# Kernel optimization log

Hardware: AMD Instinct MI355X
Metric: run time of the kernel (lower is better)

## Reference

```python
import jax, jax.numpy as jnp
import numpy as np

B, N = 8, 2048
D_IN, D_FEAT, H, K = 2, 30, 64, 8
D_ATT = D_IN + D_FEAT + H  # 96, per-head attention input dim
ALPHA = 0.2
NEG = -1e9


def setup_inputs() -> dict:
    key = jax.random.key(0)
    ks = jax.random.split(key, 11)
    inputs = jax.random.normal(ks[0], (B, N, D_IN), jnp.float32)
    envs_feat = jax.random.normal(ks[1], (B, N, D_FEAT), jnp.float32)
    state_t = jax.random.normal(ks[2], (B, N, H), jnp.float32)
    conn = jax.random.uniform(ks[3], (N, N)) < 0.05
    conn = conn | jnp.eye(N, dtype=bool)
    bias_mat = jnp.where(conn, 0.0, NEG).astype(jnp.float32)
    # xavier-ish init (gain 1.414)
    def xav(k, shape, fi, fo):
        lim = 1.414 * np.sqrt(6.0 / (fi + fo))
        return jax.random.uniform(k, shape, jnp.float32, -lim, lim)
    W_h = xav(ks[4], (K, D_ATT, H), D_ATT, H)      # stacked per-head W
    a1_h = xav(ks[5], (K, H), H, 1)
    a2_h = xav(ks[6], (K, H), H, 1)
    W_o = xav(ks[7], (K * H, H), K * H, H)
    a1_o = xav(ks[8], (H,), H, 1)
    a2_o = xav(ks[9], (H,), H, 1)
    return {"inputs": inputs, "envs_feat": envs_feat, "state_t": state_t,
            "bias_mat": bias_mat, "W_h": W_h, "a1_h": a1_h, "a2_h": a2_h,
            "W_o": W_o, "a1_o": a1_o, "a2_o": a2_o}


def _gat_multihead(h, bias, W, a1, a2):
    # h: [b,n,d], W: [k,d,h], a1/a2: [k,h], bias: [n,n]
    Wh = jnp.einsum('bnd,kdh->bknh', h, W)
    f1 = jnp.einsum('bknh,kh->bkn', Wh, a1)
    f2 = jnp.einsum('bknh,kh->bkn', Wh, a2)
    e = jax.nn.leaky_relu(f1[:, :, :, None] + f2[:, :, None, :], ALPHA) + bias  # [b,k,n,n]
    att = jax.nn.softmax(e, axis=-1)
    return jnp.einsum('bknm,bkmh->bknh', att, Wh)  # [b,k,n,h]


def _gat_single(h, bias, W, a1, a2):
    # h: [b,n,d], W: [d,h], a1/a2: [h]
    Wh = jnp.einsum('bnd,dh->bnh', h, W)
    f1 = Wh @ a1  # [b,n]
    f2 = Wh @ a2
    e = jax.nn.leaky_relu(f1[:, :, None] + f2[:, None, :], ALPHA) + bias  # [b,n,n]
    att = jax.nn.softmax(e, axis=-1)
    return jnp.einsum('bnm,bmh->bnh', att, Wh)


def reference(inputs, envs_feat, state_t, bias_mat, W_h, a1_h, a2_h, W_o, a1_o, a2_o):
    b, n = inputs.shape[0], inputs.shape[1]
    h = jnp.concatenate([inputs, envs_feat, state_t], axis=2)  # [b,n,D_ATT]
    hp = _gat_multihead(h, bias_mat, W_h, a1_h, a2_h)          # [b,k,n,h]
    h1 = jax.nn.elu(hp)
    h1 = jnp.transpose(h1, (0, 2, 1, 3)).reshape(b, n, -1)     # concat heads: [b,n,k*h]
    out = jax.nn.elu(_gat_single(h1, bias_mat, W_o, a1_o, a2_o))
    return out
```

## Files before the change

kernel.cpp:

```cpp
#include <hip/hip_runtime.h>
#include <hip/hip_bf16.h>
#include <math.h>

#define B   8
#define N   2048
#define DIN 2
#define DF  30
#define HH  64
#define KK  8
#define DATT 96
#define CAP 384
#define CAPL 176
#define ALPHA 0.2f

__device__ __forceinline__ float lrelu(float x) { return x > 0.f ? x : ALPHA * x; }
__device__ __forceinline__ float elu1(float x)  { return x > 0.f ? x : (__expf(x) - 1.f); }
__device__ __forceinline__ unsigned short f2bf(float x) {
    __hip_bfloat16 h = __float2bfloat16(x);
    return *reinterpret_cast<unsigned short*>(&h);
}
__device__ __forceinline__ float bflo(unsigned int u) { return __int_as_float(u << 16); }
__device__ __forceinline__ float bfhi(unsigned int u) { return __int_as_float(u & 0xffff0000u); }

__global__ void k_mask(const float* __restrict__ bias, int* __restrict__ cols,
                       int* __restrict__ cnt) {
    int i = blockIdx.x;
    int lane = threadIdx.x;
    int c = 0;
    for (int j0 = 0; j0 < N; j0 += 64) {
        float v = bias[(size_t)i * N + j0 + lane];
        bool conn = v > -1e8f;
        unsigned long long m = __ballot(conn);
        if (conn) {
            int pos = c + __popcll(m & ((1ull << lane) - 1ull));
            if (pos < CAP) cols[i * CAP + pos] = j0 + lane;
        }
        c += __popcll(m);
    }
    if (lane == 0) cnt[i] = c < CAP ? c : CAP;
}

__global__ void k_wh(const float* __restrict__ inp, const float* __restrict__ envs,
                     const float* __restrict__ st,  const float* __restrict__ W_h,
                     const float* __restrict__ a1,  const float* __restrict__ a2,
                     unsigned short* __restrict__ Whb,
                     float* __restrict__ f1n, float* __restrict__ f2n) {
    __shared__ float Ws[DATT * HH];
    __shared__ float hs[16 * 98];
    int k = blockIdx.y, b = blockIdx.z;
    int i0 = blockIdx.x * 16;
    int tid = threadIdx.x, lane = tid & 63, w = tid >> 6;
    int g = lane >> 4, sub = lane & 15;
    int r = w * 4 + g;

    const float* Wk = W_h + k * DATT * HH;
    for (int idx = tid * 4; idx < DATT * HH; idx += 1024)
        *(float4*)&Ws[idx] = *(const float4*)&Wk[idx];
    {
        int row = tid >> 4, q = tid & 15;
        float4 v = *(const float4*)&st[(size_t)(b * N + i0 + row) * HH + q * 4];
        float* hb = &hs[row * 98 + DIN + DF + q * 4];
        hb[0] = v.x; hb[1] = v.y; hb[2] = v.z; hb[3] = v.w;
    }
    if (tid < 240) {
        int row = tid / 15, q = tid % 15;
        float2 v = *(const float2*)&envs[(size_t)(b * N + i0 + row) * DF + q * 2];
        float* hb = &hs[row * 98 + DIN + q * 2];
        hb[0] = v.x; hb[1] = v.y;
    }
    if (tid < 32) {
        int row = tid >> 1, q = tid & 1;
        hs[row * 98 + q] = inp[(size_t)(b * N + i0 + row) * DIN + q];
    }
    __syncthreads();

    const float* hb = &hs[r * 98];
    float4 acc = make_float4(0.f, 0.f, 0.f, 0.f);
#pragma unroll
    for (int d = 0; d < DATT; d += 2) {
        float2 hv = *(const float2*)&hb[d];
        float4 w0 = *(const float4*)&Ws[d * HH + sub * 4];
        float4 w1 = *(const float4*)&Ws[(d + 1) * HH + sub * 4];
        acc.x += hv.x * w0.x; acc.y += hv.x * w0.y;
        acc.z += hv.x * w0.z; acc.w += hv.x * w0.w;
        acc.x += hv.y * w1.x; acc.y += hv.y * w1.y;
        acc.z += hv.y * w1.z; acc.w += hv.y * w1.w;
    }
    int i = i0 + r;
    unsigned int lo = (unsigned)f2bf(acc.x) | ((unsigned)f2bf(acc.y) << 16);
    unsigned int hi = (unsigned)f2bf(acc.z) | ((unsigned)f2bf(acc.w) << 16);
    *(uint2*)&Whb[((size_t)(b * N + i)) * (KK * HH) + k * HH + sub * 4] = make_uint2(lo, hi);
    float4 a1v = *(const float4*)&a1[k * HH + sub * 4];
    float4 a2v = *(const float4*)&a2[k * HH + sub * 4];
    float p1 = acc.x * a1v.x + acc.y * a1v.y + acc.z * a1v.z + acc.w * a1v.w;
    float p2 = acc.x * a2v.x + acc.y * a2v.y + acc.z * a2v.z + acc.w * a2v.w;
#pragma unroll
    for (int off = 8; off; off >>= 1) {
        p1 += __shfl_xor(p1, off);
        p2 += __shfl_xor(p2, off);
    }
    if (sub == 0) {
        f1n[((size_t)(b * N + i)) * KK + k] = p1;
        f2n[((size_t)(b * N + i)) * KK + k] = p2;
    }
}

__global__ void k_attn(const unsigned short* __restrict__ Whb, const float* __restrict__ f1n,
                       const float* __restrict__ f2n, const int* __restrict__ cols,
                       const int* __restrict__ cnt, float* __restrict__ h1) {
    __shared__ unsigned short swb[4][CAPL + 8][8];
    __shared__ int jl[4][CAPL];
    int flat = blockIdx.y * (N / 4) + blockIdx.x;
    int b = flat & 7, tile = flat >> 3;
    int tid = threadIdx.x, lane = tid & 63, w = tid >> 6;
    int i = tile * 4 + w;
    int k = lane >> 3, q = lane & 7;

    int c = cnt[i]; if (c > CAPL) c = CAPL;
    const int* cl = cols + (size_t)i * CAP;
    for (int e = lane; e < c; e += 64) jl[w][e] = cl[e];

    float f1k = f1n[((size_t)(b * N + i)) * KK + k];
    const float* f2b = f2n + (size_t)b * N * KK;

    float s[22];
    float mk = -1e30f;
#pragma unroll
    for (int t = 0; t < 22; ++t) {
        int e = t * 8 + q;
        int ee = e < c ? e : c - 1;
        int j = jl[w][ee];
        float sc = lrelu(f1k + f2b[j * KK + k]);
        if (e >= c) sc = -1e30f;
        s[t] = sc;
        mk = fmaxf(mk, sc);
    }
#pragma unroll
    for (int off = 4; off; off >>= 1) mk = fmaxf(mk, __shfl_xor(mk, off));

    float Zk = 0.f;
#pragma unroll
    for (int t = 0; t < 22; ++t) {
        float wt = __expf(s[t] - mk);
        Zk += wt;
        swb[w][t * 8 + q][k] = f2bf(wt);
    }
#pragma unroll
    for (int off = 4; off; off >>= 1) Zk += __shfl_xor(Zk, off);
    float invZ = 1.f / Zk;

    const char* Wp = (const char*)Whb + (size_t)b * N * 1024;
    float4 aL = make_float4(0.f, 0.f, 0.f, 0.f);
    float4 aH = make_float4(0.f, 0.f, 0.f, 0.f);
    int lane16 = lane << 4;
#pragma unroll 8
    for (int e = 0; e < c; ++e) {
        int j = __builtin_amdgcn_readfirstlane(jl[w][e]);
        float wt = __int_as_float((unsigned)swb[w][e][k] << 16);
        uint4 v = *(const uint4*)(Wp + ((size_t)j << 10) + lane16);
        aL.x += wt * bflo(v.x); aL.y += wt * bfhi(v.x);
        aL.z += wt * bflo(v.y); aL.w += wt * bfhi(v.y);
        aH.x += wt * bflo(v.z); aH.y += wt * bfhi(v.z);
        aH.z += wt * bflo(v.w); aH.w += wt * bfhi(v.w);
    }
    float4 o1, o2;
    o1.x = elu1(aL.x * invZ); o1.y = elu1(aL.y * invZ);
    o1.z = elu1(aL.z * invZ); o1.w = elu1(aL.w * invZ);
    o2.x = elu1(aH.x * invZ); o2.y = elu1(aH.y * invZ);
    o2.z = elu1(aH.z * invZ); o2.w = elu1(aH.w * invZ);
    float* hp = &h1[((size_t)(b * N + i)) * (KK * HH) + lane * 8];
    *(float4*)hp = o1;
    *(float4*)(hp + 4) = o2;
}

__global__ void k_who(const float* __restrict__ h1, const float* __restrict__ W_o,
                      const float* __restrict__ a1o, const float* __restrict__ a2o,
                      float* __restrict__ Who, float* __restrict__ f1o,
                      float* __restrict__ f2o) {
    __shared__ float Ws[128 * HH];
    int tid = threadIdx.x, lane = tid & 63, w = tid >> 6;
    int g = lane >> 4, sub = lane & 15;
    int row = blockIdx.x * 16 + w * 4 + g;
    const float* hp = h1 + (size_t)row * (KK * HH);
    float4 acc = make_float4(0.f, 0.f, 0.f, 0.f);
    for (int ph = 0; ph < 4; ++ph) {
        __syncthreads();
        for (int idx = tid * 4; idx < 128 * HH; idx += 1024)
            *(float4*)&Ws[idx] = *(const float4*)&W_o[ph * 128 * HH + idx];
        __syncthreads();
#pragma unroll 4
        for (int d0 = 0; d0 < 128; d0 += 4) {
            float4 hv = *(const float4*)(hp + ph * 128 + d0);
#pragma unroll
            for (int dd = 0; dd < 4; ++dd) {
                float hsv = dd == 0 ? hv.x : dd == 1 ? hv.y : dd == 2 ? hv.z : hv.w;
                float4 wv = *(const float4*)&Ws[(d0 + dd) * HH + sub * 4];
                acc.x += hsv * wv.x; acc.y += hsv * wv.y;
                acc.z += hsv * wv.z; acc.w += hsv * wv.w;
            }
        }
    }
    *(float4*)&Who[(size_t)row * HH + sub * 4] = acc;
    float4 a1v = *(const float4*)&a1o[sub * 4];
    float4 a2v = *(const float4*)&a2o[sub * 4];
    float p1 = acc.x * a1v.x + acc.y * a1v.y + acc.z * a1v.z + acc.w * a1v.w;
    float p2 = acc.x * a2v.x + acc.y * a2v.y + acc.z * a2v.z + acc.w * a2v.w;
#pragma unroll
    for (int off = 8; off; off >>= 1) {
        p1 += __shfl_xor(p1, off);
        p2 += __shfl_xor(p2, off);
    }
    if (sub == 0) { f1o[row] = p1; f2o[row] = p2; }
}

__global__ void k_attn2(const float* __restrict__ Who, const float* __restrict__ f1o,
                        const float* __restrict__ f2o, const int* __restrict__ cols,
                        const int* __restrict__ cnt, float* __restrict__ out) {
    __shared__ float2 sedge[16][CAPL + 2];
    int flat = blockIdx.y * 128 + blockIdx.x;
    int b = flat & 7;
    int tile = flat >> 3;
    int tid = threadIdx.x;
    int lane = tid & 63, w = tid >> 6;
    int g = lane >> 4, sub = lane & 15;
    int r = w * 4 + g;
    int i = tile * 16 + r;

    int c = cnt[i]; if (c > CAPL) c = CAPL;
    float f1i = f1o[b * N + i];
    const int* cl = cols + (size_t)i * CAP;
    const float* f2p = f2o + (size_t)b * N;

    float m = -1e30f;
    for (int e = sub; e < c; e += 16) {
        int j = cl[e];
        float sc = lrelu(f1i + f2p[j]);
        sedge[r][e] = make_float2(__int_as_float(j << 8), sc);
        m = fmaxf(m, sc);
    }
#pragma unroll
    for (int off = 8; off; off >>= 1) m = fmaxf(m, __shfl_xor(m, off));

    float Z = 0.f;
    for (int e = sub; e < c; e += 16) {
        float wt = __expf(sedge[r][e].y - m);
        sedge[r][e].y = wt;
        Z += wt;
    }
#pragma unroll
    for (int off = 8; off; off >>= 1) Z += __shfl_xor(Z, off);
    float invZ = 1.f / Z;

    const char* Wp = (const char*)(Who + (size_t)b * N * HH);
    int lane4 = sub << 4;
    float4 acc = make_float4(0.f, 0.f, 0.f, 0.f);
    int e = 0;
    for (; e + 4 <= c; e += 4) {
        float2 p0 = sedge[r][e];
        float2 p1 = sedge[r][e + 1];
        float2 p2 = sedge[r][e + 2];
        float2 p3 = sedge[r][e + 3];
        float4 v0 = *(const float4*)(Wp + (__float_as_int(p0.x) + lane4));
        float4 v1 = *(const float4*)(Wp + (__float_as_int(p1.x) + lane4));
        float4 v2 = *(const float4*)(Wp + (__float_as_int(p2.x) + lane4));
        float4 v3 = *(const float4*)(Wp + (__float_as_int(p3.x) + lane4));
        acc.x += p0.y * v0.x; acc.y += p0.y * v0.y;
        acc.z += p0.y * v0.z; acc.w += p0.y * v0.w;
        acc.x += p1.y * v1.x; acc.y += p1.y * v1.y;
        acc.z += p1.y * v1.z; acc.w += p1.y * v1.w;
        acc.x += p2.y * v2.x; acc.y += p2.y * v2.y;
        acc.z += p2.y * v2.z; acc.w += p2.y * v2.w;
        acc.x += p3.y * v3.x; acc.y += p3.y * v3.y;
        acc.z += p3.y * v3.z; acc.w += p3.y * v3.w;
    }
    for (; e < c; ++e) {
        float2 p0 = sedge[r][e];
        float4 v0 = *(const float4*)(Wp + (__float_as_int(p0.x) + lane4));
        acc.x += p0.y * v0.x; acc.y += p0.y * v0.y;
        acc.z += p0.y * v0.z; acc.w += p0.y * v0.w;
    }
    float4 o;
    o.x = elu1(acc.x * invZ); o.y = elu1(acc.y * invZ);
    o.z = elu1(acc.z * invZ); o.w = elu1(acc.w * invZ);
    *(float4*)&out[(size_t)(b * N + i) * HH + sub * 4] = o;
}

extern "C" void kernel_launch(void* const* d_in, const int* in_sizes, int n_in,
                              void* d_out, int out_size, void* d_ws, size_t ws_size,
                              hipStream_t stream) {
    const float* inp   = (const float*)d_in[0];
    const float* envs  = (const float*)d_in[1];
    const float* st    = (const float*)d_in[2];
    const float* bias  = (const float*)d_in[3];
    const float* W_h   = (const float*)d_in[4];
    const float* a1_h  = (const float*)d_in[5];
    const float* a2_h  = (const float*)d_in[6];
    const float* W_o   = (const float*)d_in[7];
    const float* a1_o  = (const float*)d_in[8];
    const float* a2_o  = (const float*)d_in[9];
    float* out = (float*)d_out;

    char* ws = (char*)d_ws;
    size_t off = 0;
    unsigned short* Whb = (unsigned short*)(ws + off); off += (size_t)B * N * KK * HH * 2;
    float* f1n = (float*)(ws + off); off += (size_t)B * N * KK * 4;
    float* f2n = (float*)(ws + off); off += (size_t)B * N * KK * 4;
    float* h1  = (float*)(ws + off); off += (size_t)B * N * KK * HH * 4;
    float* Who = (float*)(ws + off); off += (size_t)B * N * HH * 4;
    float* f1o = (float*)(ws + off); off += (size_t)B * N * 4;
    float* f2o = (float*)(ws + off); off += (size_t)B * N * 4;
    int*   cols = (int*)(ws + off);  off += (size_t)N * CAP * 4;
    int*   cnt  = (int*)(ws + off);  off += (size_t)N * 4;

    k_mask<<<dim3(N), dim3(64), 0, stream>>>(bias, cols, cnt);
    k_wh<<<dim3(N / 16, KK, B), dim3(256), 0, stream>>>(inp, envs, st, W_h, a1_h, a2_h,
                                                        Whb, f1n, f2n);
    k_attn<<<dim3(N / 4, B), dim3(256), 0, stream>>>(Whb, f1n, f2n, cols, cnt, h1);
    k_who<<<dim3(B * N / 16), dim3(256), 0, stream>>>(h1, W_o, a1_o, a2_o, Who, f1o, f2o);
    k_attn2<<<dim3(N / 16, B), dim3(256), 0, stream>>>(Who, f1o, f2o, cols, cnt, out);
}
```

Before: 275.1 us.

## Pack mask rows per block, keep W_h in registers, use packed FMA in attention

k_mask now handles four rows per 256-thread block instead of one row per 64-thread block. k_wh drops the shared-memory W tile: each lane holds one output column of W_h (96 floats) in registers and loops over 32 rows per block, with a wave-wide shuffle reduction for f1/f2. The attention gather accumulates with 2-wide float vectors through elementwise FMA so the compiler can emit packed FMA instructions. The changes aim to cut launch count, LDS traffic and ALU issue slots, at the cost of heavier register pressure in k_wh and more serialized rows per wave.

Measured after the change: 276.3 us. No clear change (+0.4%).

```diff
diff --git a/kernel.cpp b/kernel.cpp
--- a/kernel.cpp
+++ b/kernel.cpp
@@ -13,6 +13,8 @@
 #define CAPL 176
 #define ALPHA 0.2f
 
+typedef float f32x2 __attribute__((ext_vector_type(2)));
+
 __device__ __forceinline__ float lrelu(float x) { return x > 0.f ? x : ALPHA * x; }
 __device__ __forceinline__ float elu1(float x)  { return x > 0.f ? x : (__expf(x) - 1.f); }
 __device__ __forceinline__ unsigned short f2bf(float x) {
@@ -24,8 +26,8 @@
 
 __global__ void k_mask(const float* __restrict__ bias, int* __restrict__ cols,
                        int* __restrict__ cnt) {
-    int i = blockIdx.x;
-    int lane = threadIdx.x;
+    int i = blockIdx.x * 4 + (threadIdx.x >> 6);
+    int lane = threadIdx.x & 63;
     int c = 0;
     for (int j0 = 0; j0 < N; j0 += 64) {
         float v = bias[(size_t)i * N + j0 + lane];
@@ -45,63 +47,65 @@
                      const float* __restrict__ a1,  const float* __restrict__ a2,
                      unsigned short* __restrict__ Whb,
                      float* __restrict__ f1n, float* __restrict__ f2n) {
-    __shared__ float Ws[DATT * HH];
-    __shared__ float hs[16 * 98];
+    __shared__ float hs[32 * 100];
     int k = blockIdx.y, b = blockIdx.z;
-    int i0 = blockIdx.x * 16;
+    int i0 = blockIdx.x * 32;
     int tid = threadIdx.x, lane = tid & 63, w = tid >> 6;
-    int g = lane >> 4, sub = lane & 15;
-    int r = w * 4 + g;
-
-    const float* Wk = W_h + k * DATT * HH;
-    for (int idx = tid * 4; idx < DATT * HH; idx += 1024)
-        *(float4*)&Ws[idx] = *(const float4*)&Wk[idx];
-    {
-        int row = tid >> 4, q = tid & 15;
+
+#pragma unroll
+    for (int rep = 0; rep < 2; ++rep) {
+        int idx = rep * 256 + tid;
+        int row = idx >> 4, q = idx & 15;
         float4 v = *(const float4*)&st[(size_t)(b * N + i0 + row) * HH + q * 4];
-        float* hb = &hs[row * 98 + DIN + DF + q * 4];
+        float* hb = &hs[row * 100 + DIN + DF + q * 4];
         hb[0] = v.x; hb[1] = v.y; hb[2] = v.z; hb[3] = v.w;
     }
-    if (tid < 240) {
-        int row = tid / 15, q = tid % 15;
-        float2 v = *(const float2*)&envs[(size_t)(b * N + i0 + row) * DF + q * 2];
-        float* hb = &hs[row * 98 + DIN + q * 2];
-        hb[0] = v.x; hb[1] = v.y;
-    }
-    if (tid < 32) {
+#pragma unroll
+    for (int rep = 0; rep < 2; ++rep) {
+        int idx = rep * 256 + tid;
+        if (idx < 480) {
+            int row = idx / 15, q = idx % 15;
+            float2 v = *(const float2*)&envs[(size_t)(b * N + i0 + row) * DF + q * 2];
+            float* hb = &hs[row * 100 + DIN + q * 2];
+            hb[0] = v.x; hb[1] = v.y;
+        }
+    }
+    if (tid < 64) {
         int row = tid >> 1, q = tid & 1;
-        hs[row * 98 + q] = inp[(size_t)(b * N + i0 + row) * DIN + q];
-    }
+        hs[row * 100 + q] = inp[(size_t)(b * N + i0 + row) * DIN + q];
+    }
+
+    const float* Wk = W_h + (size_t)k * DATT * HH + lane;
+    float Wv[DATT];
+#pragma unroll
+    for (int d = 0; d < DATT; ++d) Wv[d] = Wk[(size_t)d * HH];
+    float a1k = a1[k * HH + lane], a2k = a2[k * HH + lane];
+
     __syncthreads();
 
-    const float* hb = &hs[r * 98];
-    float4 acc = make_float4(0.f, 0.f, 0.f, 0.f);
-#pragma unroll
-    for (int d = 0; d < DATT; d += 2) {
-        float2 hv = *(const float2*)&hb[d];
-        float4 w0 = *(const float4*)&Ws[d * HH + sub * 4];
-        float4 w1 = *(const float4*)&Ws[(d + 1) * HH + sub * 4];
-        acc.x += hv.x * w0.x; acc.y += hv.x * w0.y;
-        acc.z += hv.x * w0.z; acc.w += hv.x * w0.w;
-        acc.x += hv.y * w1.x; acc.y += hv.y * w1.y;
-        acc.z += hv.y * w1.z; acc.w += hv.y * w1.w;
-    }
-    int i = i0 + r;
-    unsigned int lo = (unsigned)f2bf(acc.x) | ((unsigned)f2bf(acc.y) << 16);
-    unsigned int hi = (unsigned)f2bf(acc.z) | ((unsigned)f2bf(acc.w) << 16);
-    *(uint2*)&Whb[((size_t)(b * N + i)) * (KK * HH) + k * HH + sub * 4] = make_uint2(lo, hi);
-    float4 a1v = *(const float4*)&a1[k * HH + sub * 4];
-    float4 a2v = *(const float4*)&a2[k * HH + sub * 4];
-    float p1 = acc.x * a1v.x + acc.y * a1v.y + acc.z * a1v.z + acc.w * a1v.w;
-    float p2 = acc.x * a2v.x + acc.y * a2v.y + acc.z * a2v.z + acc.w * a2v.w;
-#pragma unroll
-    for (int off = 8; off; off >>= 1) {
-        p1 += __shfl_xor(p1, off);
-        p2 += __shfl_xor(p2, off);
-    }
-    if (sub == 0) {
-        f1n[((size_t)(b * N + i)) * KK + k] = p1;
-        f2n[((size_t)(b * N + i)) * KK + k] = p2;
+    for (int rr = 0; rr < 8; ++rr) {
+        int r = w * 8 + rr;
+        const float* hb = &hs[r * 100];
+        float acc0 = 0.f, acc1 = 0.f;
+#pragma unroll
+        for (int d = 0; d < DATT; d += 2) {
+            float2 hv = *(const float2*)&hb[d];
+            acc0 += hv.x * Wv[d];
+            acc1 += hv.y * Wv[d + 1];
+        }
+        float acc = acc0 + acc1;
+        int i = i0 + r;
+        Whb[((size_t)(b * N + i)) * (KK * HH) + k * HH + lane] = f2bf(acc);
+        float p1 = acc * a1k, p2 = acc * a2k;
+#pragma unroll
+        for (int off = 32; off; off >>= 1) {
+            p1 += __shfl_xor(p1, off);
+            p2 += __shfl_xor(p2, off);
+        }
+        if (lane == 0) {
+            f1n[((size_t)(b * N + i)) * KK + k] = p1;
+            f2n[((size_t)(b * N + i)) * KK + k] = p2;
+        }
     }
 }
 
@@ -150,24 +154,28 @@
     float invZ = 1.f / Zk;
 
     const char* Wp = (const char*)Whb + (size_t)b * N * 1024;
-    float4 aL = make_float4(0.f, 0.f, 0.f, 0.f);
-    float4 aH = make_float4(0.f, 0.f, 0.f, 0.f);
+    f32x2 a0 = {0.f, 0.f}, a1_ = {0.f, 0.f}, a2_ = {0.f, 0.f}, a3 = {0.f, 0.f};
     int lane16 = lane << 4;
 #pragma unroll 8
     for (int e = 0; e < c; ++e) {
         int j = __builtin_amdgcn_readfirstlane(jl[w][e]);
         float wt = __int_as_float((unsigned)swb[w][e][k] << 16);
+        f32x2 wt2 = {wt, wt};
         uint4 v = *(const uint4*)(Wp + ((size_t)j << 10) + lane16);
-        aL.x += wt * bflo(v.x); aL.y += wt * bfhi(v.x);
-        aL.z += wt * bflo(v.y); aL.w += wt * bfhi(v.y);
-        aH.x += wt * bflo(v.z); aH.y += wt * bfhi(v.z);
-        aH.z += wt * bflo(v.w); aH.w += wt * bfhi(v.w);
+        f32x2 v0 = {bflo(v.x), bfhi(v.x)};
+        f32x2 v1 = {bflo(v.y), bfhi(v.y)};
+        f32x2 v2 = {bflo(v.z), bfhi(v.z)};
+        f32x2 v3 = {bflo(v.w), bfhi(v.w)};
+        a0 = __builtin_elementwise_fma(wt2, v0, a0);
+        a1_ = __builtin_elementwise_fma(wt2, v1, a1_);
+        a2_ = __builtin_elementwise_fma(wt2, v2, a2_);
+        a3 = __builtin_elementwise_fma(wt2, v3, a3);
     }
     float4 o1, o2;
-    o1.x = elu1(aL.x * invZ); o1.y = elu1(aL.y * invZ);
-    o1.z = elu1(aL.z * invZ); o1.w = elu1(aL.w * invZ);
-    o2.x = elu1(aH.x * invZ); o2.y = elu1(aH.y * invZ);
-    o2.z = elu1(aH.z * invZ); o2.w = elu1(aH.w * invZ);
+    o1.x = elu1(a0.x * invZ); o1.y = elu1(a0.y * invZ);
+    o1.z = elu1(a1_.x * invZ); o1.w = elu1(a1_.y * invZ);
+    o2.x = elu1(a2_.x * invZ); o2.y = elu1(a2_.y * invZ);
+    o2.z = elu1(a3.x * invZ); o2.w = elu1(a3.y * invZ);
     float* hp = &h1[((size_t)(b * N + i)) * (KK * HH) + lane * 8];
     *(float4*)hp = o1;
     *(float4*)(hp + 4) = o2;
@@ -312,8 +320,8 @@
     int*   cols = (int*)(ws + off);  off += (size_t)N * CAP * 4;
     int*   cnt  = (int*)(ws + off);  off += (size_t)N * 4;
 
-    k_mask<<<dim3(N), dim3(64), 0, stream>>>(bias, cols, cnt);
-    k_wh<<<dim3(N / 16, KK, B), dim3(256), 0, stream>>>(inp, envs, st, W_h, a1_h, a2_h,
+    k_mask<<<dim3(N / 4), dim3(256), 0, stream>>>(bias, cols, cnt);
+    k_wh<<<dim3(N / 32, KK, B), dim3(256), 0, stream>>>(inp, envs, st, W_h, a1_h, a2_h,
                                                         Whb, f1n, f2n);
     k_attn<<<dim3(N / 4, B), dim3(256), 0, stream>>>(Whb, f1n, f2n, cols, cnt, h1);
     k_who<<<dim3(B * N / 16), dim3(256), 0, stream>>>(h1, W_o, a1_o, a2_o, Who, f1o, f2o);
```
